# Kernel optimization log

Hardware: AMD Instinct MI355X
Metric: run time of the kernel (lower is better)

Reference implementation:

```python
import jax, jax.numpy as jnp
import numpy as np

B = 524288      # batch
F = 32          # nr_features
C = 10          # nr_classes
H = 64          # hidden_size
D = 2           # tree_depth
NN = 2 ** D - 1 # internal nodes
NL = 2 ** D     # leaf nodes
EPS = 1e-5

# Static tree routing tables, reproducing the original Python int() (truncate-toward-zero) math exactly.
NODE_IDX = np.array([[int((2 ** (d - 1) * (2 ** D + l) - 2 ** D) / 2 ** D) for d in range(D)] for l in range(NL)])  # [NL, D]
PSIGN = np.array([[int(l / 2 ** (D - d)) % 2 for d in range(D)] for l in range(NL)])  # [NL, D]


def _linear_params(key, out_f, in_f):
    k1, k2 = jax.random.split(key)
    bound = 1.0 / np.sqrt(in_f)
    w = jax.random.uniform(k1, (out_f, in_f), minval=-bound, maxval=bound, dtype=jnp.float32)
    b = jax.random.uniform(k2, (out_f,), minval=-bound, maxval=bound, dtype=jnp.float32)
    return w, b


def setup_inputs() -> dict:
    key = jax.random.key(0)
    ks = jax.random.split(key, 6)
    x = jax.random.normal(ks[0], (B, F), dtype=jnp.float32)
    w_in, b_in = _linear_params(ks[1], H, F)
    bn_g = jnp.ones((H,), dtype=jnp.float32)   # BatchNorm1d weight init to 1
    bn_b = jnp.zeros((H,), dtype=jnp.float32)  # BatchNorm1d bias init to 0
    w_fi, b_fi = _linear_params(ks[2], NN * F, H)
    w_fs, b_fs = _linear_params(ks[3], NN * F, H)
    w_lc, b_lc = _linear_params(ks[4], NL * C, H)
    return {"x": x, "w_in": w_in, "b_in": b_in, "bn_g": bn_g, "bn_b": bn_b,
            "w_fi": w_fi, "b_fi": b_fi, "w_fs": w_fs, "b_fs": b_fs,
            "w_lc": w_lc, "b_lc": b_lc}


def reference(x, w_in, b_in, bn_g, bn_b, w_fi, b_fi, w_fs, b_fs, w_lc, b_lc):
    inp = x  # raw features used inside the tree gating
    # input layer + BatchNorm1d (training-mode batch stats, biased var) + exact GELU
    h = x @ w_in.T + b_in                                   # [B, H]
    mu = jnp.mean(h, axis=0)
    var = jnp.var(h, axis=0)
    h = (h - mu) / jnp.sqrt(var + EPS) * bn_g + bn_b
    h = jax.nn.gelu(h, approximate=False)

    fi = (h @ w_fi.T + b_fi).reshape(B, NN, F)              # feature importances per node
    fs = (h @ w_fs.T + b_fs).reshape(B, NN, F)              # feature splits per node
    lc = (h @ w_lc.T + b_lc).reshape(B, NL, C)              # leaf class logits

    smx = jax.nn.softmax(fi, axis=-1)                        # [B, NN, F]
    # node_sd = sigmoid(sum(smx*input) - sum(smx*fs))
    sd = jax.nn.sigmoid(jnp.einsum('bnf,bnf->bn', smx, inp[:, None, :] - fs))  # [B, NN]

    # gate per (leaf, depth): sd if p==0 else 1-sd, at the statically-computed node index
    g = sd[:, NODE_IDX]                                      # [B, NL, D]
    g = jnp.where(PSIGN[None, :, :] == 0, g, 1.0 - g)
    coeff = jnp.prod(g, axis=-1)                             # [B, NL]

    out = jnp.einsum('blc,bl->bc', lc, coeff)                # [B, C]
    return out
```

## Files before the change

### kernel.cpp

```cpp
#include <hip/hip_runtime.h>

typedef __attribute__((ext_vector_type(8))) __bf16 bf16x8;
typedef __attribute__((ext_vector_type(4))) float f32x4;
typedef unsigned short u16;
typedef unsigned int u32;

#define NB 524288
#define HSS 72
#define EPSI 1e-5f

__device__ __forceinline__ float bf2f(u16 h) {
    union { u32 u; float f; } cv; cv.u = ((u32)h) << 16; return cv.f;
}
__device__ __forceinline__ u16 f2bf(float f) {
    __bf16 b = (__bf16)f; return __builtin_bit_cast(u16, b);
}
__device__ __forceinline__ float ldany(const void* p, long i, int isf) {
    return isf ? ((const float*)p)[i] : bf2f(((const u16*)p)[i]);
}

__device__ __forceinline__ float fast_gelu(float v) {
    float t = 1.5957691216057308f * v * (1.0f + 0.044715f * v * v);
    float en = __expf(-t);
    return v * __builtin_amdgcn_rcpf(1.0f + en);
}

__device__ __forceinline__ bf16x8 loadfrag(const __bf16* p) {
    return *reinterpret_cast<const bf16x8*>(p);
}
__device__ __forceinline__ bf16x8 loadfrag(const float* p) {
    f32x4 a = *reinterpret_cast<const f32x4*>(p);
    f32x4 b = *reinterpret_cast<const f32x4*>(p + 4);
    bf16x8 r;
#pragma unroll
    for (int i = 0; i < 4; ++i) { r[i] = (__bf16)a[i]; r[4 + i] = (__bf16)b[i]; }
    return r;
}

__device__ __forceinline__ int detect_isf(const void* x) {
    const int lane = threadIdx.x & 63;
    u32 w0 = ((const u32*)x)[lane];
    u32 w1 = ((const u32*)x)[64 + lane];
    int hit = ((((w0 >> 7) & 0xFFu) >= 0xC0u) || (((w1 >> 7) & 0xFFu) >= 0xC0u)) ? 1 : 0;
    return __ballot(hit) != 0ull;
}

template<typename T>
__device__ __forceinline__ void stats_body(const T* __restrict__ x,
                                           const T* __restrict__ w_in,
                                           float* __restrict__ ws,
                                           float* __restrict__ red) {
    const int lane = threadIdx.x & 63;
    const int wave = threadIdx.x >> 6;
    const int c = lane & 15;
    const int q = lane >> 4;

    bf16x8 b1[4];
#pragma unroll
    for (int nt = 0; nt < 4; ++nt)
        b1[nt] = loadfrag(w_in + (nt * 16 + c) * 32 + q * 8);

    float accs[4][4], accq[4][4];
#pragma unroll
    for (int nt = 0; nt < 4; ++nt)
#pragma unroll
        for (int r = 0; r < 4; ++r) { accs[nt][r] = 0.f; accq[nt][r] = 0.f; }

    const int wid = blockIdx.x * 4 + wave;
    for (int t = 0; t < 8; ++t) {
        const long row0 = ((long)wid * 8 + t) * 16;
        bf16x8 a1 = loadfrag(x + (row0 + c) * 32 + q * 8);
#pragma unroll
        for (int nt = 0; nt < 4; ++nt) {
            f32x4 z = {0.f, 0.f, 0.f, 0.f};
            f32x4 acc = __builtin_amdgcn_mfma_f32_16x16x32_bf16(a1, b1[nt], z, 0, 0, 0);
#pragma unroll
            for (int r = 0; r < 4; ++r) {
                float v = acc[r];
                accs[nt][r] += v;
                accq[nt][r] += v * v;
            }
        }
    }
    for (int i = threadIdx.x; i < 128; i += 256) red[i] = 0.f;
    __syncthreads();
#pragma unroll
    for (int nt = 0; nt < 4; ++nt) {
        float s  = accs[nt][0] + accs[nt][1] + accs[nt][2] + accs[nt][3];
        float sq = accq[nt][0] + accq[nt][1] + accq[nt][2] + accq[nt][3];
        s  += __shfl_xor(s, 16);  s  += __shfl_xor(s, 32);
        sq += __shfl_xor(sq, 16); sq += __shfl_xor(sq, 32);
        if (q == 0) {
            atomicAdd(&red[nt * 16 + c], s);
            atomicAdd(&red[64 + nt * 16 + c], sq);
        }
    }
    __syncthreads();
    for (int i = threadIdx.x; i < 128; i += 256) atomicAdd(&ws[i], red[i]);
}

__global__ __launch_bounds__(256) void stats_kernel(
    const void* x, const void* w_in, const void* w_fi, const void* b_fi,
    const void* w_fs, const void* b_fs, const void* w_lc, const void* b_lc,
    float* __restrict__ ws)
{
    const int isf = detect_isf(x);

    if (blockIdx.x < 24) {
        u16* W2p = (u16*)(ws + 384);
        const int idx = blockIdx.x * 256 + threadIdx.x;
        const int g = idx >> 6, f = idx & 63;
        float v = 0.f;
        if (g < 32)                 v = ldany(w_fi, (long)g * 64 + f, isf);
        else if (g < 64)            v = ldany(w_fs, (long)(g - 32) * 64 + f, isf);
        else if (g < 74)            v = ldany(w_lc, (long)(g - 64) * 64 + f, isf)
                                      + ldany(w_lc, (long)(g - 54) * 64 + f, isf);
        else if (g >= 80 && g < 90) v = ldany(w_lc, (long)(g - 60) * 64 + f, isf)
                                      + ldany(w_lc, (long)(g - 50) * 64 + f, isf);
        W2p[idx] = f2bf(v);
    } else if (blockIdx.x == 24 && threadIdx.x < 96) {
        float* biasP = ws + 288;
        const int g = threadIdx.x;
        float v = 0.f;
        if (g < 32)                 v = ldany(b_fi, g, isf);
        else if (g < 64)            v = ldany(b_fs, g - 32, isf);
        else if (g < 74)            v = ldany(b_lc, g - 64, isf) + ldany(b_lc, g - 54, isf);
        else if (g >= 80 && g < 90) v = ldany(b_lc, g - 60, isf) + ldany(b_lc, g - 50, isf);
        biasP[g] = v;
    }

    __shared__ float red[128];
    if (isf) stats_body<float>((const float*)x, (const float*)w_in, ws, red);
    else     stats_body<__bf16>((const __bf16*)x, (const __bf16*)w_in, ws, red);
}

template<typename T>
__device__ __forceinline__ void main_body(
    const T* __restrict__ x, const T* __restrict__ bn_g, const T* __restrict__ bn_b,
    const T* __restrict__ w_in, const float* __restrict__ ws,
    T* __restrict__ out, __bf16* __restrict__ hs0, __bf16* __restrict__ hs1)
{
    const int lane = threadIdx.x & 63;
    const int c = lane & 15;
    const int q = lane >> 4;
    const float* biasP = ws + 288;
    const u16* W2p = (const u16*)(ws + 384);

    bf16x8 b1[4];
#pragma unroll
    for (int nt = 0; nt < 4; ++nt)
        b1[nt] = loadfrag(w_in + (nt * 16 + c) * 32 + q * 8);

    bf16x8 b2[6][2];
#pragma unroll
    for (int nt = 0; nt < 6; ++nt)
#pragma unroll
        for (int kt = 0; kt < 2; ++kt)
            b2[nt][kt] = *reinterpret_cast<const bf16x8*>(W2p + (nt * 16 + c) * 64 + kt * 32 + q * 8);

    float scale_r[4], shift_r[4];
#pragma unroll
    for (int nt = 0; nt < 4; ++nt) {
        int j = nt * 16 + c;
        float mu  = ws[j] * (1.0f / NB);
        float var = fmaxf(ws[64 + j] * (1.0f / NB) - mu * mu, 0.0f);
        float s = (float)bn_g[j] * rsqrtf(var + EPSI);
        scale_r[nt] = s;
        shift_r[nt] = (float)bn_b[j] - mu * s;
    }

    const float bfi0 = biasP[c],      bfi1 = biasP[16 + c];
    const float bfs0 = biasP[32 + c], bfs1 = biasP[48 + c];
    const float bu   = biasP[64 + c], bv   = biasP[80 + c];

    const long wid = blockIdx.x;
#pragma unroll 2
    for (int t = 0; t < 8; ++t) {
        __bf16* hs = (t & 1) ? hs1 : hs0;
        const long row0 = wid * 128 + (long)t * 16;
        bf16x8 a1 = loadfrag(x + (row0 + c) * 32 + q * 8);

        float xv0[4], xv1[4];
#pragma unroll
        for (int r = 0; r < 4; ++r) {
            xv0[r] = (float)x[(row0 + q * 4 + r) * 32 + c];
            xv1[r] = (float)x[(row0 + q * 4 + r) * 32 + 16 + c];
        }

        f32x4 h4[4];
#pragma unroll
        for (int nt = 0; nt < 4; ++nt) {
            f32x4 z = {0.f, 0.f, 0.f, 0.f};
            h4[nt] = __builtin_amdgcn_mfma_f32_16x16x32_bf16(a1, b1[nt], z, 0, 0, 0);
        }
#pragma unroll
        for (int nt = 0; nt < 4; ++nt)
#pragma unroll
            for (int r = 0; r < 4; ++r) {
                float v = h4[nt][r] * scale_r[nt] + shift_r[nt];
                hs[(q * 4 + r) * HSS + nt * 16 + c] = (__bf16)fast_gelu(v);
            }
        __asm__ volatile("" ::: "memory");

        bf16x8 a2_0 = *reinterpret_cast<const bf16x8*>(hs + c * HSS + q * 8);
        bf16x8 a2_1 = *reinterpret_cast<const bf16x8*>(hs + c * HSS + 32 + q * 8);

        f32x4 acc[6];
#pragma unroll
        for (int nt = 0; nt < 6; ++nt) {
            f32x4 z = {0.f, 0.f, 0.f, 0.f};
            acc[nt] = __builtin_amdgcn_mfma_f32_16x16x32_bf16(a2_0, b2[nt][0], z, 0, 0, 0);
            acc[nt] = __builtin_amdgcn_mfma_f32_16x16x32_bf16(a2_1, b2[nt][1], acc[nt], 0, 0, 0);
        }

#pragma unroll
        for (int r = 0; r < 4; ++r) {
            float e0  = __expf(acc[0][r] + bfi0);
            float e1  = __expf(acc[1][r] + bfi1);
            float fs0 = acc[2][r] + bfs0;
            float fs1 = acc[3][r] + bfs1;
            float es = e0 + e1;
            float dp = e0 * (xv0[r] - fs0) + e1 * (xv1[r] - fs1);
#pragma unroll
            for (int m = 1; m < 16; m <<= 1) {
                es += __shfl_xor(es, m);
                dp += __shfl_xor(dp, m);
            }
            float d  = dp * __builtin_amdgcn_rcpf(es);
            float sd = __builtin_amdgcn_rcpf(1.0f + __expf(-d));
            float uu = acc[4][r] + bu, vv = acc[5][r] + bv;
            float o = sd * (vv + sd * (uu - vv));
            if (c < 10) out[(row0 + q * 4 + r) * 10 + c] = (T)o;
        }
        __asm__ volatile("" ::: "memory");
    }
}

__global__ __launch_bounds__(64, 4) void main_kernel(
    const void* x, const void* bn_g, const void* bn_b, const void* w_in,
    float* ws, void* outv)
{
    __shared__ __attribute__((aligned(16))) __bf16 hs0[16 * HSS];
    __shared__ __attribute__((aligned(16))) __bf16 hs1[16 * HSS];
    if (detect_isf(x))
        main_body<float>((const float*)x, (const float*)bn_g, (const float*)bn_b,
                         (const float*)w_in, ws, (float*)outv, hs0, hs1);
    else
        main_body<__bf16>((const __bf16*)x, (const __bf16*)bn_g, (const __bf16*)bn_b,
                          (const __bf16*)w_in, ws, (__bf16*)outv, hs0, hs1);
}

extern "C" void kernel_launch(void* const* d_in, const int* in_sizes, int n_in,
                              void* d_out, int out_size, void* d_ws, size_t ws_size,
                              hipStream_t stream) {
    float* ws = (float*)d_ws;
    hipMemsetAsync(d_ws, 0, 512, stream);
    stats_kernel<<<1024, 256, 0, stream>>>(d_in[0], d_in[1], d_in[5], d_in[6],
                                           d_in[7], d_in[8], d_in[9], d_in[10], ws);
    main_kernel<<<4096, 64, 0, stream>>>(d_in[0], d_in[3], d_in[4], d_in[1], ws, d_out);
}
```

Baseline: 180.8 us.

## Keep hidden activations in registers via transposed MFMA and permuted weight rows

The first GEMM is computed transposed with the input weight rows permuted, so each lane's MFMA output already sits in the A-operand layout the second GEMM needs. This removes the LDS round trip for the hidden activations. BatchNorm scale is folded into the bf16 weights, shuffle reductions become DPP row rotates, and the launch uses 256-thread blocks of four independent waves. Folding the scale into bf16 weights before rounding slightly changes numerics.

```diff
diff --git a/kernel.cpp b/kernel.cpp
--- a/kernel.cpp
+++ b/kernel.cpp
@@ -6,7 +6,6 @@
 typedef unsigned int u32;
 
 #define NB 524288
-#define HSS 72
 #define EPSI 1e-5f
 
 __device__ __forceinline__ float bf2f(u16 h) {
@@ -23,6 +22,22 @@
     float t = 1.5957691216057308f * v * (1.0f + 0.044715f * v * v);
     float en = __expf(-t);
     return v * __builtin_amdgcn_rcpf(1.0f + en);
+}
+
+template<typename T>
+__device__ __forceinline__ void load8f(const T* p, float* o);
+template<>
+__device__ __forceinline__ void load8f<__bf16>(const __bf16* p, float* o) {
+    bf16x8 r = *reinterpret_cast<const bf16x8*>(p);
+#pragma unroll
+    for (int i = 0; i < 8; ++i) o[i] = (float)r[i];
+}
+template<>
+__device__ __forceinline__ void load8f<float>(const float* p, float* o) {
+    f32x4 a = *reinterpret_cast<const f32x4*>(p);
+    f32x4 b = *reinterpret_cast<const f32x4*>(p + 4);
+#pragma unroll
+    for (int i = 0; i < 4; ++i) { o[i] = a[i]; o[4 + i] = b[i]; }
 }
 
 __device__ __forceinline__ bf16x8 loadfrag(const __bf16* p) {
@@ -43,6 +58,19 @@
     u32 w1 = ((const u32*)x)[64 + lane];
     int hit = ((((w0 >> 7) & 0xFFu) >= 0xC0u) || (((w1 >> 7) & 0xFFu) >= 0xC0u)) ? 1 : 0;
     return __ballot(hit) != 0ull;
+}
+
+template<int CTRL>
+__device__ __forceinline__ float dpp_rot_add(float v) {
+    int s = __builtin_amdgcn_update_dpp(0, __builtin_bit_cast(int, v), CTRL, 0xF, 0xF, false);
+    return v + __builtin_bit_cast(float, s);
+}
+__device__ __forceinline__ float row_reduce_add(float v) {
+    v = dpp_rot_add<0x121>(v);
+    v = dpp_rot_add<0x122>(v);
+    v = dpp_rot_add<0x124>(v);
+    v = dpp_rot_add<0x128>(v);
+    return v;
 }
 
 template<typename T>
@@ -137,10 +165,10 @@
 template<typename T>
 __device__ __forceinline__ void main_body(
     const T* __restrict__ x, const T* __restrict__ bn_g, const T* __restrict__ bn_b,
-    const T* __restrict__ w_in, const float* __restrict__ ws,
-    T* __restrict__ out, __bf16* __restrict__ hs0, __bf16* __restrict__ hs1)
+    const T* __restrict__ w_in, const float* __restrict__ ws, T* __restrict__ out)
 {
     const int lane = threadIdx.x & 63;
+    const int wave = threadIdx.x >> 6;
     const int c = lane & 15;
     const int q = lane >> 4;
     const float* biasP = ws + 288;
@@ -148,8 +176,30 @@
 
     bf16x8 b1[4];
 #pragma unroll
+    for (int nt = 0; nt < 4; ++nt) {
+        const int row = 32 * (nt >> 1) + 8 * (c >> 2) + 4 * (nt & 1) + (c & 3);
+        float mu  = ws[row] * (1.0f / NB);
+        float var = fmaxf(ws[64 + row] * (1.0f / NB) - mu * mu, 0.0f);
+        float s   = (float)bn_g[row] * rsqrtf(var + EPSI);
+        float w8[8];
+        load8f(w_in + row * 32 + q * 8, w8);
+        bf16x8 f;
+#pragma unroll
+        for (int j = 0; j < 8; ++j) f[j] = (__bf16)(w8[j] * s);
+        b1[nt] = f;
+    }
+
+    float shift_t[4][4];
+#pragma unroll
     for (int nt = 0; nt < 4; ++nt)
-        b1[nt] = loadfrag(w_in + (nt * 16 + c) * 32 + q * 8);
+#pragma unroll
+        for (int r = 0; r < 4; ++r) {
+            const int ft = 32 * (nt >> 1) + 8 * q + 4 * (nt & 1) + r;
+            float mu  = ws[ft] * (1.0f / NB);
+            float var = fmaxf(ws[64 + ft] * (1.0f / NB) - mu * mu, 0.0f);
+            float s   = (float)bn_g[ft] * rsqrtf(var + EPSI);
+            shift_t[nt][r] = (float)bn_b[ft] - mu * s;
+        }
 
     bf16x8 b2[6][2];
 #pragma unroll
@@ -157,27 +207,15 @@
 #pragma unroll
         for (int kt = 0; kt < 2; ++kt)
             b2[nt][kt] = *reinterpret_cast<const bf16x8*>(W2p + (nt * 16 + c) * 64 + kt * 32 + q * 8);
-
-    float scale_r[4], shift_r[4];
-#pragma unroll
-    for (int nt = 0; nt < 4; ++nt) {
-        int j = nt * 16 + c;
-        float mu  = ws[j] * (1.0f / NB);
-        float var = fmaxf(ws[64 + j] * (1.0f / NB) - mu * mu, 0.0f);
-        float s = (float)bn_g[j] * rsqrtf(var + EPSI);
-        scale_r[nt] = s;
-        shift_r[nt] = (float)bn_b[j] - mu * s;
-    }
 
     const float bfi0 = biasP[c],      bfi1 = biasP[16 + c];
     const float bfs0 = biasP[32 + c], bfs1 = biasP[48 + c];
     const float bu   = biasP[64 + c], bv   = biasP[80 + c];
 
-    const long wid = blockIdx.x;
+    const long gw = (long)blockIdx.x * 4 + wave;
 #pragma unroll 2
     for (int t = 0; t < 8; ++t) {
-        __bf16* hs = (t & 1) ? hs1 : hs0;
-        const long row0 = wid * 128 + (long)t * 16;
+        const long row0 = gw * 128 + (long)t * 16;
         bf16x8 a1 = loadfrag(x + (row0 + c) * 32 + q * 8);
 
         float xv0[4], xv1[4];
@@ -191,19 +229,17 @@
 #pragma unroll
         for (int nt = 0; nt < 4; ++nt) {
             f32x4 z = {0.f, 0.f, 0.f, 0.f};
-            h4[nt] = __builtin_amdgcn_mfma_f32_16x16x32_bf16(a1, b1[nt], z, 0, 0, 0);
-        }
-#pragma unroll
-        for (int nt = 0; nt < 4; ++nt)
+            h4[nt] = __builtin_amdgcn_mfma_f32_16x16x32_bf16(b1[nt], a1, z, 0, 0, 0);
+        }
+
+        bf16x8 a2_0, a2_1;
+#pragma unroll
+        for (int nt = 0; nt < 2; ++nt)
 #pragma unroll
             for (int r = 0; r < 4; ++r) {
-                float v = h4[nt][r] * scale_r[nt] + shift_r[nt];
-                hs[(q * 4 + r) * HSS + nt * 16 + c] = (__bf16)fast_gelu(v);
+                a2_0[nt * 4 + r] = (__bf16)fast_gelu(h4[nt][r] + shift_t[nt][r]);
+                a2_1[nt * 4 + r] = (__bf16)fast_gelu(h4[2 + nt][r] + shift_t[2 + nt][r]);
             }
-        __asm__ volatile("" ::: "memory");
-
-        bf16x8 a2_0 = *reinterpret_cast<const bf16x8*>(hs + c * HSS + q * 8);
-        bf16x8 a2_1 = *reinterpret_cast<const bf16x8*>(hs + c * HSS + 32 + q * 8);
 
         f32x4 acc[6];
 #pragma unroll
@@ -219,35 +255,27 @@
             float e1  = __expf(acc[1][r] + bfi1);
             float fs0 = acc[2][r] + bfs0;
             float fs1 = acc[3][r] + bfs1;
-            float es = e0 + e1;
-            float dp = e0 * (xv0[r] - fs0) + e1 * (xv1[r] - fs1);
-#pragma unroll
-            for (int m = 1; m < 16; m <<= 1) {
-                es += __shfl_xor(es, m);
-                dp += __shfl_xor(dp, m);
-            }
+            float es = row_reduce_add(e0 + e1);
+            float dp = row_reduce_add(e0 * (xv0[r] - fs0) + e1 * (xv1[r] - fs1));
             float d  = dp * __builtin_amdgcn_rcpf(es);
             float sd = __builtin_amdgcn_rcpf(1.0f + __expf(-d));
             float uu = acc[4][r] + bu, vv = acc[5][r] + bv;
             float o = sd * (vv + sd * (uu - vv));
             if (c < 10) out[(row0 + q * 4 + r) * 10 + c] = (T)o;
         }
-        __asm__ volatile("" ::: "memory");
-    }
-}
-
-__global__ __launch_bounds__(64, 4) void main_kernel(
+    }
+}
+
+__global__ __launch_bounds__(256, 4) void main_kernel(
     const void* x, const void* bn_g, const void* bn_b, const void* w_in,
     float* ws, void* outv)
 {
-    __shared__ __attribute__((aligned(16))) __bf16 hs0[16 * HSS];
-    __shared__ __attribute__((aligned(16))) __bf16 hs1[16 * HSS];
     if (detect_isf(x))
         main_body<float>((const float*)x, (const float*)bn_g, (const float*)bn_b,
-                         (const float*)w_in, ws, (float*)outv, hs0, hs1);
+                         (const float*)w_in, ws, (float*)outv);
     else
         main_body<__bf16>((const __bf16*)x, (const __bf16*)bn_g, (const __bf16*)bn_b,
-                          (const __bf16*)w_in, ws, (__bf16*)outv, hs0, hs1);
+                          (const __bf16*)w_in, ws, (__bf16*)outv);
 }
 
 extern "C" void kernel_launch(void* const* d_in, const int* in_sizes, int n_in,
@@ -257,5 +285,5 @@
     hipMemsetAsync(d_ws, 0, 512, stream);
     stats_kernel<<<1024, 256, 0, stream>>>(d_in[0], d_in[1], d_in[5], d_in[6],
                                            d_in[7], d_in[8], d_in[9], d_in[10], ws);
-    main_kernel<<<4096, 64, 0, stream>>>(d_in[0], d_in[3], d_in[4], d_in[1], ws, d_out);
-}
+    main_kernel<<<1024, 256, 0, stream>>>(d_in[0], d_in[3], d_in[4], d_in[1], ws, d_out);
+}
```

New measurement: 176.7 us. 2.3% less time.
